# Performance work log

Measured on AMD Instinct MI355X. Metric: run time of the kernel, lower is better.

## Reference

```python
import jax, jax.numpy as jnp
import numpy as np

EMBED_DIM = 1024
NUM_HEADS = 16
HEAD_DIM = EMBED_DIM // NUM_HEADS


def setup_inputs() -> dict:
    key = jax.random.key(0)
    ks = jax.random.split(key, 9)
    B, S, D = 2, 2048, EMBED_DIM
    scale = 1.0 / np.sqrt(D)
    inp = {
        "x": jax.random.normal(ks[0], (B, S, D), dtype=jnp.float32),
        "w_q": jax.random.normal(ks[1], (D, D), dtype=jnp.float32) * scale,
        "b_q": jnp.zeros((D,), dtype=jnp.float32),
        "w_k": jax.random.normal(ks[2], (D, D), dtype=jnp.float32) * scale,
        "b_k": jnp.zeros((D,), dtype=jnp.float32),
        "w_v": jax.random.normal(ks[3], (D, D), dtype=jnp.float32) * scale,
        "b_v": jnp.zeros((D,), dtype=jnp.float32),
        "w_o": jax.random.normal(ks[4], (D, D), dtype=jnp.float32) * scale,
        "b_o": jnp.zeros((D,), dtype=jnp.float32),
    }
    return inp


def reference(x, w_q, b_q, w_k, b_k, w_v, b_v, w_o, b_o):
    B, S, D = x.shape
    H, Hd = NUM_HEADS, HEAD_DIM

    def proj(w, b):
        # (B,S,D) @ (D,D) -> (B,S,D) -> (B,H,S,Hd)
        y = jnp.einsum('bsd,df->bsf', x, w) + b
        return y.reshape(B, S, H, Hd).transpose(0, 2, 1, 3)

    q = proj(w_q, b_q)
    k = proj(w_k, b_k)
    v = proj(w_v, b_v)

    scores = jnp.einsum('bhqd,bhkd->bhqk', q, k) / jnp.sqrt(jnp.float32(Hd))
    attn = jax.nn.softmax(scores, axis=-1)
    context = jnp.einsum('bhqk,bhkd->bhqd', attn, v)
    context = context.transpose(0, 2, 1, 3).reshape(B, S, D)
    return jnp.einsum('bsd,df->bsf', context + x, w_o) + b_o
```

## Files before the change

### kernel.cpp

```cpp
#include <hip/hip_runtime.h>
#include <hip/hip_bf16.h>

typedef _Float16 f16;
typedef _Float16 f16x8 __attribute__((ext_vector_type(8)));
typedef _Float16 f16x4 __attribute__((ext_vector_type(4)));
typedef float f32x4 __attribute__((ext_vector_type(4)));

#define EMBED 1024
#define NHEAD 16
#define HDIM 64
#define SEQ 2048
#define BATCH 2
#define NROW (BATCH * SEQ)
#define PSTR 72
#define PBYTES (64 * PSTR * 2)
#define MBIAS 14.4269504089f
#define QSCALE 0.1803368801f

__device__ __forceinline__ void gld_lds16(const f16* g, f16* l) {
    __builtin_amdgcn_global_load_lds(
        (const __attribute__((address_space(1))) void*)g,
        (__attribute__((address_space(3))) void*)l, 16, 0, 0);
}

__global__ void k_prep(const float* __restrict__ wq, const float* __restrict__ wk,
                       const float* __restrict__ wv, const float* __restrict__ wo,
                       const float* __restrict__ x,
                       f16* __restrict__ wqkvt, f16* __restrict__ wot, f16* __restrict__ xb) {
    if (blockIdx.z >= 4) {
        int i = (((blockIdx.z - 4) * 1024 + blockIdx.y * 32 + blockIdx.x) * 256 + threadIdx.x) * 4;
        float4 v = *(const float4*)&x[i];
        f16x4 o = {(f16)v.x, (f16)v.y, (f16)v.z, (f16)v.w};
        *(f16x4*)&xb[i] = o;
        return;
    }
    const float* W;
    f16* Wt;
    switch (blockIdx.z) {
        case 0: W = wq; Wt = wqkvt; break;
        case 1: W = wk; Wt = wqkvt + 1024 * 1024; break;
        case 2: W = wv; Wt = wqkvt + 2 * 1024 * 1024; break;
        default: W = wo; Wt = wot; break;
    }
    __shared__ float t[32][33];
    int tx = threadIdx.x & 31, ty = threadIdx.x >> 5;
    int r0 = blockIdx.y * 32, c0 = blockIdx.x * 32;
    for (int j = 0; j < 4; ++j)
        t[ty + j * 8][tx] = W[(r0 + ty + j * 8) * 1024 + c0 + tx];
    __syncthreads();
    for (int j = 0; j < 4; ++j)
        Wt[(c0 + ty + j * 8) * 1024 + r0 + tx] = (f16)t[tx][ty + j * 8];
}

__global__ void k_bias(const float* __restrict__ bq, const float* __restrict__ bk,
                       const float* __restrict__ bv, float* __restrict__ bias) {
    int i = blockIdx.x * blockDim.x + threadIdx.x;
    if (i < 3072) bias[i] = (i < 1024) ? bq[i] : ((i < 2048) ? bk[i - 1024] : bv[i - 2048]);
}

template <bool SWAP>
__device__ __forceinline__ void gemm_kloop(const f16* __restrict__ A, const f16* __restrict__ Bt,
                                           int K, f16* Al, f16* Bl, int m0, int n0,
                                           int w, int quad, int l16, int mw, int nw,
                                           int crow, int ccol, f32x4 (&acc)[4][4]) {
    for (int k0 = 0; k0 < K; k0 += 32) {
        __syncthreads();
        gld_lds16(&A[(m0 + crow) * K + k0 + ccol], &Al[(w * 64) * 8]);
        gld_lds16(&A[(m0 + 64 + crow) * K + k0 + ccol], &Al[(256 + w * 64) * 8]);
        gld_lds16(&Bt[(n0 + crow) * K + k0 + ccol], &Bl[(w * 64) * 8]);
        gld_lds16(&Bt[(n0 + 64 + crow) * K + k0 + ccol], &Bl[(256 + w * 64) * 8]);
        __syncthreads();
        f16x8 af[4], bf[4];
        for (int i = 0; i < 4; ++i)
            af[i] = *(const f16x8*)&Al[(mw + i * 16 + l16) * 32 + quad * 8];
        for (int j = 0; j < 4; ++j)
            bf[j] = *(const f16x8*)&Bl[(nw + j * 16 + l16) * 32 + quad * 8];
        for (int i = 0; i < 4; ++i)
            for (int j = 0; j < 4; ++j)
                acc[i][j] = SWAP
                    ? __builtin_amdgcn_mfma_f32_16x16x32_f16(bf[j], af[i], acc[i][j], 0, 0, 0)
                    : __builtin_amdgcn_mfma_f32_16x16x32_f16(af[i], bf[j], acc[i][j], 0, 0, 0);
    }
}

__global__ __launch_bounds__(256) void k_gemm_qkv(const f16* __restrict__ A, const f16* __restrict__ Bt,
                                                  const float* __restrict__ bias,
                                                  f16* __restrict__ qk, f16* __restrict__ Vt) {
    __shared__ __align__(16) f16 Al[128 * 32];
    __shared__ __align__(16) f16 Bl[128 * 32];
    const int K = 1024;
    int tid = threadIdx.x;
    int w = tid >> 6, lane = tid & 63, quad = lane >> 4, l16 = lane & 15;
    int m0 = blockIdx.x * 128, n0 = blockIdx.y * 128;
    int mw = (w >> 1) * 64, nw = (w & 1) * 64;
    int c = w * 64 + lane;
    int crow = c >> 2, ccol = (c & 3) * 8;
    f32x4 acc[4][4] = {};

    if (n0 >= 2048) {
        gemm_kloop<true>(A, Bt, K, Al, Bl, m0, n0, w, quad, l16, mw, nw, crow, ccol, acc);
        for (int i = 0; i < 4; ++i) {
            int mrow = m0 + mw + i * 16 + l16;
            int b = mrow >> 11, s = mrow & 2047;
            for (int j = 0; j < 4; ++j)
                for (int r = 0; r < 4; ++r) {
                    int col = n0 + nw + j * 16 + quad * 4 + r;
                    int d = col - 2048;
                    Vt[(b * 1024 + d) * SEQ + s] = (f16)(acc[i][j][r] + bias[col]);
                }
        }
    } else {
        gemm_kloop<false>(A, Bt, K, Al, Bl, m0, n0, w, quad, l16, mw, nw, crow, ccol, acc);
        for (int i = 0; i < 4; ++i) {
            int row = m0 + mw + i * 16 + quad * 4;
            for (int j = 0; j < 4; ++j) {
                int col = n0 + nw + j * 16 + l16;
                float bval = bias[col];
                for (int r = 0; r < 4; ++r)
                    qk[(row + r) * 2048 + col] = (f16)(acc[i][j][r] + bval);
            }
        }
    }
}

__global__ __launch_bounds__(256) void k_gemm_out(const f16* __restrict__ A, const f16* __restrict__ Bt,
                                                  const float* __restrict__ bias, float* __restrict__ Cout) {
    __shared__ __align__(16) f16 Al[128 * 32];
    __shared__ __align__(16) f16 Bl[64 * 32];
    const int K = 1024, N = 1024;
    int tid = threadIdx.x;
    int w = tid >> 6, lane = tid & 63, quad = lane >> 4, l16 = lane & 15;
    int m0 = blockIdx.x * 128, n0 = blockIdx.y * 64;
    int mw = (w >> 1) * 64, nw = (w & 1) * 32;
    int c = w * 64 + lane;
    int crow = c >> 2, ccol = (c & 3) * 8;
    f32x4 acc[4][2] = {};

    for (int k0 = 0; k0 < K; k0 += 32) {
        __syncthreads();
        gld_lds16(&A[(m0 + crow) * K + k0 + ccol], &Al[(w * 64) * 8]);
        gld_lds16(&A[(m0 + 64 + crow) * K + k0 + ccol], &Al[(256 + w * 64) * 8]);
        gld_lds16(&Bt[(n0 + crow) * K + k0 + ccol], &Bl[(w * 64) * 8]);
        __syncthreads();
        f16x8 af[4], bf[2];
        for (int i = 0; i < 4; ++i)
            af[i] = *(const f16x8*)&Al[(mw + i * 16 + l16) * 32 + quad * 8];
        for (int j = 0; j < 2; ++j)
            bf[j] = *(const f16x8*)&Bl[(nw + j * 16 + l16) * 32 + quad * 8];
        for (int i = 0; i < 4; ++i)
            for (int j = 0; j < 2; ++j)
                acc[i][j] = __builtin_amdgcn_mfma_f32_16x16x32_f16(af[i], bf[j], acc[i][j], 0, 0, 0);
    }

    for (int i = 0; i < 4; ++i) {
        int row = m0 + mw + i * 16 + quad * 4;
        for (int j = 0; j < 2; ++j) {
            int col = n0 + nw + j * 16 + l16;
            float bval = bias[col];
            for (int r = 0; r < 4; ++r)
                Cout[(row + r) * N + col] = acc[i][j][r] + bval;
        }
    }
}

__global__ __launch_bounds__(256, 2) void k_attn(const f16* __restrict__ qk, const f16* __restrict__ Vt,
                                                 const float* __restrict__ x, f16* __restrict__ ctx) {
    __shared__ __align__(16) char smem[4 * PBYTES];

    int tid = threadIdx.x;
    int w = tid >> 6, lane = tid & 63, quad = lane >> 4, l16 = lane & 15;
    int q0 = blockIdx.x * 64;
    int bh = blockIdx.y, b = bh >> 4, h = bh & 15;
    int kbase = 1024 + h * 64;
    int qcol = h * 64;
    int vbase = b * 1024 + h * 64;

    f16* Kw = (f16*)(smem + w * PBYTES);
    f16* Pw = Kw;

    f16x8 qf[4][2];
    for (int qg = 0; qg < 4; ++qg) {
        int qrow = b * SEQ + q0 + qg * 16 + l16;
        for (int kk = 0; kk < 2; ++kk) {
            f16x8 v = *(const f16x8*)&qk[qrow * 2048 + qcol + kk * 32 + quad * 8];
            for (int e = 0; e < 8; ++e) v[e] = (f16)((float)v[e] * QSCALE);
            qf[qg][kk] = v;
        }
    }

    int srow = lane >> 3;
    int scol = (lane & 7) * 8;
    const f16* kgp = &qk[(b * SEQ + w * 512 + srow) * 2048 + kbase + scol];
    const f16* vfp = &Vt[(vbase + l16) * SEQ + w * 512 + quad * 8];

    f32x4 oacc[4][4] = {};
    float li[4] = {0.f, 0.f, 0.f, 0.f};

    for (int kt = 0; kt < 8; ++kt) {
        f16x8 tk[8];
        for (int c = 0; c < 8; ++c)
            tk[c] = *(const f16x8*)(kgp + c * 8 * 2048);
        kgp += 64 * 2048;
        for (int c = 0; c < 8; ++c)
            *(f16x8*)&Kw[(c * 8 + srow) * PSTR + scol] = tk[c];

        f16x8 kf[4][2];
        for (int nt = 0; nt < 4; ++nt)
            for (int kk = 0; kk < 2; ++kk)
                kf[nt][kk] = *(const f16x8*)&Kw[(nt * 16 + l16) * PSTR + kk * 32 + quad * 8];
        asm volatile("s_waitcnt lgkmcnt(0)" ::: "memory");

        for (int qg = 0; qg < 4; ++qg) {
            f32x4 st[4];
            for (int nt = 0; nt < 4; ++nt) {
                f32x4 s = {};
                s = __builtin_amdgcn_mfma_f32_16x16x32_f16(kf[nt][0], qf[qg][0], s, 0, 0, 0);
                s = __builtin_amdgcn_mfma_f32_16x16x32_f16(kf[nt][1], qf[qg][1], s, 0, 0, 0);
                st[nt] = s;
            }
            float rs = 0.f;
            for (int nt = 0; nt < 4; ++nt)
                for (int r = 0; r < 4; ++r) {
                    float p = __builtin_amdgcn_exp2f(st[nt][r] - MBIAS);
                    st[nt][r] = p;
                    rs += p;
                }
            rs += __shfl_xor(rs, 16);
            rs += __shfl_xor(rs, 32);
            li[qg] += rs;
            for (int nt = 0; nt < 4; ++nt) {
                f16x4 pk;
                for (int r = 0; r < 4; ++r) pk[r] = (f16)st[nt][r];
                *(f16x4*)&Pw[(qg * 16 + l16) * PSTR + nt * 16 + quad * 4] = pk;
            }
        }
        asm volatile("s_waitcnt lgkmcnt(0)" ::: "memory");

        f16x8 pf[4][2];
        for (int qg = 0; qg < 4; ++qg)
            for (int kk = 0; kk < 2; ++kk)
                pf[qg][kk] = *(const f16x8*)&Pw[(qg * 16 + l16) * PSTR + kk * 32 + quad * 8];
        for (int nt = 0; nt < 4; ++nt) {
            f16x8 vf0 = *(const f16x8*)(vfp + nt * 16 * SEQ);
            f16x8 vf1 = *(const f16x8*)(vfp + nt * 16 * SEQ + 32);
            for (int qg = 0; qg < 4; ++qg) {
                oacc[qg][nt] = __builtin_amdgcn_mfma_f32_16x16x32_f16(pf[qg][0], vf0, oacc[qg][nt], 0, 0, 0);
                oacc[qg][nt] = __builtin_amdgcn_mfma_f32_16x16x32_f16(pf[qg][1], vf1, oacc[qg][nt], 0, 0, 0);
            }
        }
        vfp += 64;
    }

    float* Ow = (float*)(smem + (w & 1) * 16640);
    float* Lw = (float*)(smem + (w & 1) * 16640 + 16384);
    __syncthreads();
    if (w < 2) {
        for (int qg = 0; qg < 4; ++qg)
            for (int nt = 0; nt < 4; ++nt)
                for (int r = 0; r < 4; ++r)
                    Ow[(qg * 16 + quad * 4 + r) * 64 + nt * 16 + l16] = oacc[qg][nt][r];
        if (quad == 0)
            for (int qg = 0; qg < 4; ++qg) Lw[qg * 16 + l16] = li[qg];
    }
    __syncthreads();
    if (w >= 2) {
        for (int qg = 0; qg < 4; ++qg)
            for (int nt = 0; nt < 4; ++nt)
                for (int r = 0; r < 4; ++r)
                    Ow[(qg * 16 + quad * 4 + r) * 64 + nt * 16 + l16] += oacc[qg][nt][r];
        if (quad == 0)
            for (int qg = 0; qg < 4; ++qg) Lw[qg * 16 + l16] += li[qg];
    }
    __syncthreads();

    int q = tid >> 2, d0 = (tid & 3) * 16;
    const float* O0 = (const float*)smem;
    const float* O1 = (const float*)(smem + 16640);
    f32x4 a4[4];
    for (int j = 0; j < 4; ++j)
        a4[j] = *(const f32x4*)&O0[q * 64 + d0 + 4 * j];
    for (int j = 0; j < 4; ++j)
        a4[j] += *(const f32x4*)&O1[q * 64 + d0 + 4 * j];
    float lsum = ((const float*)(smem + 16384))[q] + ((const float*)(smem + 16640 + 16384))[q];

    int g = b * SEQ + q0 + q;
    int cb = h * 64 + d0;
    float inv = 1.f / lsum;
    f16x8 o0, o1;
    for (int j = 0; j < 4; ++j) {
        float4 xv = *(const float4*)&x[g * 1024 + cb + 4 * j];
        float4 r;
        r.x = a4[j][0] * inv + xv.x;
        r.y = a4[j][1] * inv + xv.y;
        r.z = a4[j][2] * inv + xv.z;
        r.w = a4[j][3] * inv + xv.w;
        f16* dst = (j < 2) ? (f16*)&o0 : (f16*)&o1;
        int o = (j & 1) * 4;
        dst[o + 0] = (f16)r.x; dst[o + 1] = (f16)r.y; dst[o + 2] = (f16)r.z; dst[o + 3] = (f16)r.w;
    }
    *(f16x8*)&ctx[g * 1024 + cb] = o0;
    *(f16x8*)&ctx[g * 1024 + cb + 8] = o1;
}

extern "C" void kernel_launch(void* const* d_in, const int* in_sizes, int n_in,
                              void* d_out, int out_size, void* d_ws, size_t ws_size,
                              hipStream_t stream) {
    const float* x  = (const float*)d_in[0];
    const float* wq = (const float*)d_in[1];
    const float* bq = (const float*)d_in[2];
    const float* wk = (const float*)d_in[3];
    const float* bk = (const float*)d_in[4];
    const float* wv = (const float*)d_in[5];
    const float* bv = (const float*)d_in[6];
    const float* wo = (const float*)d_in[7];
    const float* bo = (const float*)d_in[8];
    float* out = (float*)d_out;

    char* ws = (char*)d_ws;
    f16*   xb    = (f16*)(ws);
    f16*   wqkvt = (f16*)(ws + (8u << 20));
    f16*   wot   = (f16*)(ws + (14u << 20));
    float* biasq = (float*)(ws + (16u << 20));
    f16*   qkbuf = (f16*)(ws + (16u << 20) + (64u << 10));
    f16*   vtbuf = (f16*)(ws + (32u << 20) + (64u << 10));
    f16*   ctx   = xb;

    k_prep<<<dim3(32, 32, 8), 256, 0, stream>>>(wq, wk, wv, wo, x, wqkvt, wot, xb);
    k_bias<<<12, 256, 0, stream>>>(bq, bk, bv, biasq);

    k_gemm_qkv<<<dim3(32, 24), 256, 0, stream>>>(xb, wqkvt, biasq, qkbuf, vtbuf);
    k_attn<<<dim3(SEQ / 64, BATCH * NHEAD), 256, 0, stream>>>(qkbuf, vtbuf, x, ctx);
    k_gemm_out<<<dim3(32, 16), 256, 0, stream>>>(ctx, wot, bo, out);
}
```

Before: 218.3 us.

## Double-buffer K tiles via async global-to-LDS loads with XOR swizzle; remap GEMM blocks

The attention kernel now streams K tiles straight into LDS with global_load_lds into two per-wave buffers. The next tile is prefetched while the current one is computed, and the padded layout is replaced by an XOR-swizzled layout to avoid bank conflicts. This removes the register round-trip and exposes load latency to overlap. Both GEMM kernels also remap block IDs to group tiles for better L2 reuse. LDS use per block doubles (64KB with two blocks per CU), which may limit occupancy, and the vmcnt(0) wait also blocks on outstanding V loads.

```diff
diff --git a/kernel.cpp b/kernel.cpp
--- a/kernel.cpp
+++ b/kernel.cpp
@@ -12,8 +12,8 @@
 #define SEQ 2048
 #define BATCH 2
 #define NROW (BATCH * SEQ)
-#define PSTR 72
-#define PBYTES (64 * PSTR * 2)
+#define KBYTES 8192
+#define WBYTES (2 * KBYTES)
 #define MBIAS 14.4269504089f
 #define QSCALE 0.1803368801f
 
@@ -91,7 +91,9 @@
     const int K = 1024;
     int tid = threadIdx.x;
     int w = tid >> 6, lane = tid & 63, quad = lane >> 4, l16 = lane & 15;
-    int m0 = blockIdx.x * 128, n0 = blockIdx.y * 128;
+    int bid = blockIdx.y * gridDim.x + blockIdx.x;
+    int t = (bid & 7) * 96 + (bid >> 3);
+    int m0 = (t & 31) * 128, n0 = (t >> 5) * 128;
     int mw = (w >> 1) * 64, nw = (w & 1) * 64;
     int c = w * 64 + lane;
     int crow = c >> 2, ccol = (c & 3) * 8;
@@ -130,7 +132,9 @@
     const int K = 1024, N = 1024;
     int tid = threadIdx.x;
     int w = tid >> 6, lane = tid & 63, quad = lane >> 4, l16 = lane & 15;
-    int m0 = blockIdx.x * 128, n0 = blockIdx.y * 64;
+    int bid = blockIdx.y * gridDim.x + blockIdx.x;
+    int t = (bid & 7) * 64 + (bid >> 3);
+    int m0 = (t & 31) * 128, n0 = (t >> 5) * 64;
     int mw = (w >> 1) * 64, nw = (w & 1) * 32;
     int c = w * 64 + lane;
     int crow = c >> 2, ccol = (c & 3) * 8;
@@ -165,7 +169,7 @@
 
 __global__ __launch_bounds__(256, 2) void k_attn(const f16* __restrict__ qk, const f16* __restrict__ Vt,
                                                  const float* __restrict__ x, f16* __restrict__ ctx) {
-    __shared__ __align__(16) char smem[4 * PBYTES];
+    __shared__ __align__(16) char smem[4 * WBYTES];
 
     int tid = threadIdx.x;
     int w = tid >> 6, lane = tid & 63, quad = lane >> 4, l16 = lane & 15;
@@ -175,8 +179,16 @@
     int qcol = h * 64;
     int vbase = b * 1024 + h * 64;
 
-    f16* Kw = (f16*)(smem + w * PBYTES);
-    f16* Pw = Kw;
+    f16* K0 = (f16*)(smem + w * WBYTES);
+    f16* K1 = K0 + KBYTES / 2;
+
+    int prow = lane >> 3;
+    int pj = (lane & 7) ^ prow;
+    const f16* kpre = &qk[(b * SEQ + w * 512 + prow) * 2048 + kbase + pj * 8];
+
+    for (int c = 0; c < 8; ++c)
+        gld_lds16(kpre + c * 8 * 2048, K0 + c * 512);
+    kpre += 64 * 2048;
 
     f16x8 qf[4][2];
     for (int qg = 0; qg < 4; ++qg) {
@@ -188,27 +200,28 @@
         }
     }
 
-    int srow = lane >> 3;
-    int scol = (lane & 7) * 8;
-    const f16* kgp = &qk[(b * SEQ + w * 512 + srow) * 2048 + kbase + scol];
     const f16* vfp = &Vt[(vbase + l16) * SEQ + w * 512 + quad * 8];
 
     f32x4 oacc[4][4] = {};
     float li[4] = {0.f, 0.f, 0.f, 0.f};
-
+    int sw = l16 & 7;
+
+    f16* Kc = K0;
+    f16* Kn = K1;
     for (int kt = 0; kt < 8; ++kt) {
-        f16x8 tk[8];
-        for (int c = 0; c < 8; ++c)
-            tk[c] = *(const f16x8*)(kgp + c * 8 * 2048);
-        kgp += 64 * 2048;
-        for (int c = 0; c < 8; ++c)
-            *(f16x8*)&Kw[(c * 8 + srow) * PSTR + scol] = tk[c];
+        asm volatile("s_waitcnt vmcnt(0)" ::: "memory");
 
         f16x8 kf[4][2];
         for (int nt = 0; nt < 4; ++nt)
             for (int kk = 0; kk < 2; ++kk)
-                kf[nt][kk] = *(const f16x8*)&Kw[(nt * 16 + l16) * PSTR + kk * 32 + quad * 8];
+                kf[nt][kk] = *(const f16x8*)&Kc[(nt * 16 + l16) * 64 + (((kk * 4 + quad) ^ sw) * 8)];
         asm volatile("s_waitcnt lgkmcnt(0)" ::: "memory");
+
+        if (kt < 7) {
+            for (int c = 0; c < 8; ++c)
+                gld_lds16(kpre + c * 8 * 2048, Kn + c * 512);
+            kpre += 64 * 2048;
+        }
 
         for (int qg = 0; qg < 4; ++qg) {
             f32x4 st[4];
@@ -228,10 +241,11 @@
             rs += __shfl_xor(rs, 16);
             rs += __shfl_xor(rs, 32);
             li[qg] += rs;
+            int row = qg * 16 + l16;
             for (int nt = 0; nt < 4; ++nt) {
                 f16x4 pk;
                 for (int r = 0; r < 4; ++r) pk[r] = (f16)st[nt][r];
-                *(f16x4*)&Pw[(qg * 16 + l16) * PSTR + nt * 16 + quad * 4] = pk;
+                *(f16x4*)&Kc[row * 64 + (((2 * nt + (quad >> 1)) ^ sw) * 8) + (quad & 1) * 4] = pk;
             }
         }
         asm volatile("s_waitcnt lgkmcnt(0)" ::: "memory");
@@ -239,7 +253,7 @@
         f16x8 pf[4][2];
         for (int qg = 0; qg < 4; ++qg)
             for (int kk = 0; kk < 2; ++kk)
-                pf[qg][kk] = *(const f16x8*)&Pw[(qg * 16 + l16) * PSTR + kk * 32 + quad * 8];
+                pf[qg][kk] = *(const f16x8*)&Kc[(qg * 16 + l16) * 64 + (((kk * 4 + quad) ^ sw) * 8)];
         for (int nt = 0; nt < 4; ++nt) {
             f16x8 vf0 = *(const f16x8*)(vfp + nt * 16 * SEQ);
             f16x8 vf1 = *(const f16x8*)(vfp + nt * 16 * SEQ + 32);
@@ -249,6 +263,7 @@
             }
         }
         vfp += 64;
+        f16* tmp = Kc; Kc = Kn; Kn = tmp;
     }
 
     float* Ow = (float*)(smem + (w & 1) * 16640);
```

Measured after the change: 220.6 us. No clear change (+1.1%).
